# Optimization experiments

Measured on AMD Instinct MI355X. Metric: run time of the kernel, lower is better.

The kernel has to match this reference:

```python
import jax, jax.numpy as jnp
import numpy as np

N = 50000   # num_node
E = 1600000 # edge_size (N * avg_degree 32)
B = 64      # batch, hardcoded via repeat(64,1,1) in the torch module


def setup_inputs() -> dict:
    key = jax.random.key(0)
    k = jax.random.split(key, 8)
    return {
        "t": jax.random.normal(k[0], (1,), dtype=jnp.float32),
        "input": jax.random.normal(k[1], (B, N), dtype=jnp.float32),
        "edge_i": jax.random.randint(k[2], (E,), 0, N, dtype=jnp.int32),
        "edge_j": jax.random.randint(k[3], (E,), 0, N, dtype=jnp.int32),
        "weight_react": jax.random.normal(k[4], (1, E), dtype=jnp.float32) / 10.0,
        "weight_diff": jax.random.normal(k[5], (1, E), dtype=jnp.float32) / 1000.0,
        "bias_reaction": jax.random.normal(k[6], (1, N), dtype=jnp.float32) / 10.0,
        "bias_diffusion": jax.random.normal(k[7], (1, N), dtype=jnp.float32) / 10.0,
    }


def _lap_matvec(x, w, src, dst, n):
    # W[src_e, dst_e] = w_e (duplicates coalesce by sum, as torch sparse_coo_tensor does)
    # L = diag(colsum(W)) - W ; returns x @ L^T applied batched: out[b, v] = (L x[b])[v]
    col = jax.ops.segment_sum(w, dst, num_segments=n)                 # [N] column sums
    msg = jax.ops.segment_sum(w[:, None] * x[:, dst].T, src,
                              num_segments=n)                          # [N, B]
    return col[None, :] * x - msg.T                                   # [B, N]


def reference(t, input, edge_i, edge_j, weight_react, weight_diff,
              bias_reaction, bias_diffusion):
    x = input                                                          # [B, N]
    n = x.shape[1]
    # reaction Laplacian uses edges (i -> j); diffusion uses transposed (j -> i)
    reaction = _lap_matvec(x, weight_react[0], edge_i, edge_j, n) + bias_reaction
    diffusion = _lap_matvec(x, weight_diff[0], edge_j, edge_i, n) + bias_diffusion
    # up and down both True: tanh(reaction) + diffusion + input
    return jnp.tanh(reaction) + diffusion + x
```

## Files before the change

### kernel.cpp

```cpp
#include <hip/hip_runtime.h>
#include <hip/hip_fp16.h>


#define BKT_SHIFT 7
#define BKT_NODES 128
#define RCAP 4608
#define RCAP2 4992
#define CH 4096
#define NBP 512

#define RFL(x) __builtin_amdgcn_readfirstlane(x)

__device__ __forceinline__ unsigned bf16_rne(float f) {
    unsigned u = __float_as_uint(f);
    unsigned rb = (u >> 16) & 1u;
    u += 0x7FFFu + rb;
    return u >> 16;
}
__device__ __forceinline__ float bf16_lo(int y) {
    return __uint_as_float(((unsigned)y) << 16);
}
__device__ __forceinline__ float bf16_hi(int y) {
    return __uint_as_float((unsigned)y & 0xFFFF0000u);
}

__global__ void transpose_kernel(const float* __restrict__ x, __half* __restrict__ xth,
                                 int* __restrict__ gcur, int ngcur, int N) {
    __shared__ float tile[64][65];
    int v0 = blockIdx.x * 64;
    int tx = threadIdx.x;
    int ty = threadIdx.y;
    int flat = blockIdx.x * 1024 + ty * 64 + tx;
    if (flat < ngcur) gcur[flat] = 0;
    if (v0 + tx < N) {
        for (int b = ty; b < 64; b += 16)
            tile[tx][b] = x[b * N + v0 + tx];
    }
    __syncthreads();
    for (int vl = ty; vl < 64; vl += 16) {
        int v = v0 + vl;
        if (v < N)
            xth[(size_t)v * 64 + tx] = __float2half(tile[vl][tx]);
    }
}

__global__ void __launch_bounds__(512) partition_kernel(
        const int* __restrict__ ei, const int* __restrict__ ej,
        const float* __restrict__ wr, const float* __restrict__ wd,
        int* __restrict__ gcur, int2* __restrict__ runs,
        int E, int NB) {
    __shared__ int cnt[2 * NBP];
    __shared__ int base_a[2 * NBP];
    __shared__ int gb[2 * NBP];
    __shared__ int2 buf[2 * CH];

    int tid = threadIdx.x;
    int e0 = blockIdx.x * CH;
    int ch_len = min(CH, E - e0);
    if (ch_len <= 0) return;

    int my_i[8], my_j[8];
    unsigned my_w[8];
    #pragma unroll
    for (int k = 0; k < 8; ++k) {
        int t = tid + k * 512;
        if (t < ch_len) {
            int e = e0 + t;
            my_i[k] = ei[e];
            my_j[k] = ej[e];
            my_w[k] = (bf16_rne(wr[e]) << 16) | bf16_rne(wd[e]);
        } else {
            my_i[k] = -1;
        }
    }

    for (int b = tid; b < 2 * NBP; b += 512) cnt[b] = 0;
    __syncthreads();
    #pragma unroll
    for (int k = 0; k < 8; ++k) {
        if (my_i[k] >= 0) {
            atomicAdd(&cnt[my_i[k] >> BKT_SHIFT], 1);
            atomicAdd(&cnt[NBP + (my_j[k] >> BKT_SHIFT)], 1);
        }
    }
    __syncthreads();
    if (tid < 64) {
        int carry = 0;
        #pragma unroll
        for (int c = 0; c < (2 * NBP) / 64; ++c) {
            int idx = c * 64 + tid;
            int val = cnt[idx];
            int scan = val;
            for (int off = 1; off < 64; off <<= 1) {
                int n = __shfl_up(scan, off, 64);
                if (tid >= off) scan += n;
            }
            int excl = scan - val + carry;
            base_a[idx] = excl;
            cnt[idx] = excl;
            carry += __shfl(scan, 63, 64);
        }
    }
    __syncthreads();
    #pragma unroll
    for (int k = 0; k < 8; ++k) {
        if (my_i[k] >= 0) {
            int i = my_i[k], j = my_j[k];
            unsigned wv = my_w[k];
            int b0 = i >> BKT_SHIFT;
            int p0 = atomicAdd(&cnt[b0], 1);
            buf[p0] = make_int2((int)(((unsigned)b0 << 23) | ((unsigned)(i & 127) << 16) | (unsigned)j),
                                (int)wv);
            int b1 = j >> BKT_SHIFT;
            int p1 = atomicAdd(&cnt[NBP + b1], 1);
            buf[p1] = make_int2((int)(((unsigned)b1 << 23) | ((unsigned)(j & 127) << 16) | (unsigned)i),
                                (int)((wv << 16) | (wv >> 16)));
        }
    }
    __syncthreads();
    for (int cb = tid; cb < 2 * NBP; cb += 512) {
        int n = cnt[cb] - base_a[cb];
        if (n > 0) {
            int side = cb >> 9;
            int bkt = cb & (NBP - 1);
            gb[cb] = atomicAdd(&gcur[side * NB + bkt], n);
        }
    }
    __syncthreads();
    int total = 2 * ch_len;
    for (int t = tid; t < total; t += 512) {
        int2 p = buf[t];
        int side = (t >= ch_len) ? 1 : 0;
        int bkt = ((unsigned)p.x >> 23) & 0x1FF;
        int cb = side * NBP + bkt;
        int rank = gb[cb] + (t - base_a[cb]);
        if (rank < RCAP)
            runs[((size_t)(side * NB + bkt)) * RCAP + rank] = p;
    }
}

__global__ void __launch_bounds__(512) sortgather_kernel(
        const int* __restrict__ gcur, const int2* __restrict__ runs,
        const __half* __restrict__ xth,
        __half* __restrict__ msg, float* __restrict__ colsum,
        int NB, int N) {
    __shared__ int cnt[BKT_NODES];
    __shared__ int cur[BKT_NODES];
    __shared__ int pb[BKT_NODES];
    __shared__ float csum[BKT_NODES];
    __shared__ int dst[RCAP2];

    int sb = blockIdx.x;
    int side = (sb >= NB) ? 1 : 0;
    int b = sb - side * NB;
    int v0 = b << BKT_SHIFT;
    int len = min(gcur[sb], RCAP);
    size_t roff = (size_t)sb * RCAP;
    int tid = threadIdx.x;

    if (tid < BKT_NODES) { cnt[tid] = 0; csum[tid] = 0.f; }
    __syncthreads();
    for (int k = tid; k < len; k += 512) {
        int2 p = runs[roff + k];
        int dl = ((unsigned)p.x >> 16) & 0x7F;
        atomicAdd(&cnt[dl], 1);
        atomicAdd(&csum[dl], bf16_lo(p.y));
    }
    __syncthreads();
    if (tid < 64) {
        int carry = 0;
        #pragma unroll
        for (int c = 0; c < BKT_NODES / 64; ++c) {
            int idx = c * 64 + tid;
            int val = (cnt[idx] + 3) & ~3;
            int scan = val;
            for (int off = 1; off < 64; off <<= 1) {
                int n = __shfl_up(scan, off, 64);
                if (tid >= off) scan += n;
            }
            int excl = scan - val + carry;
            pb[idx] = excl;
            cur[idx] = excl;
            carry += __shfl(scan, 63, 64);
        }
    }
    __syncthreads();
    if (tid < BKT_NODES) {
        int pc = (cnt[tid] + 3) & ~3;
        for (int t = cnt[tid]; t < pc; ++t) dst[pb[tid] + t] = 0;
    }
    __syncthreads();
    for (int k = tid; k < len; k += 512) {
        int2 p = runs[roff + k];
        int dl = ((unsigned)p.x >> 16) & 0x7F;
        int pos = atomicAdd(&cur[dl], 1);
        dst[pos] = (int)(((unsigned)p.y & 0xFFFF0000u) | ((unsigned)p.x & 0xFFFFu));
    }
    __syncthreads();

    const unsigned* __restrict__ xth2 = (const unsigned*)xth;
    int lane = tid & 63;
    int halfl = lane & 31;
    int hi = lane >> 5;
    int wid = tid >> 6;
    for (int t = 0; t < BKT_NODES / 8; ++t) {
        int dl = wid * (BKT_NODES / 8) + t;
        int v = v0 + dl;
        if (v >= N) continue;
        const int* pay = dst + pb[dl] + hi;
        int npair = ((cnt[dl] + 3) & ~3) >> 1;
        float a0 = 0.f, a1 = 0.f;
        int q = 0;
        for (; q + 4 <= npair; q += 4) {
            int pA = pay[2 * q];
            int pB = pay[2 * q + 2];
            int pC = pay[2 * q + 4];
            int pD = pay[2 * q + 6];
            unsigned dA = xth2[(((size_t)((unsigned)pA & 0xFFFFu)) << 5) + halfl];
            unsigned dB = xth2[(((size_t)((unsigned)pB & 0xFFFFu)) << 5) + halfl];
            unsigned dC = xth2[(((size_t)((unsigned)pC & 0xFFFFu)) << 5) + halfl];
            unsigned dD = xth2[(((size_t)((unsigned)pD & 0xFFFFu)) << 5) + halfl];
            float wA = bf16_hi(pA), wB = bf16_hi(pB);
            float wC = bf16_hi(pC), wD = bf16_hi(pD);
            float2 xA = __half22float2(*(const __half2*)&dA);
            float2 xB = __half22float2(*(const __half2*)&dB);
            float2 xC = __half22float2(*(const __half2*)&dC);
            float2 xD = __half22float2(*(const __half2*)&dD);
            a0 = fmaf(wA, xA.x, a0); a1 = fmaf(wA, xA.y, a1);
            a0 = fmaf(wB, xB.x, a0); a1 = fmaf(wB, xB.y, a1);
            a0 = fmaf(wC, xC.x, a0); a1 = fmaf(wC, xC.y, a1);
            a0 = fmaf(wD, xD.x, a0); a1 = fmaf(wD, xD.y, a1);
        }
        for (; q < npair; ++q) {
            int p = pay[2 * q];
            unsigned d = xth2[(((size_t)((unsigned)p & 0xFFFFu)) << 5) + halfl];
            float wv = bf16_hi(p);
            float2 xf = __half22float2(*(const __half2*)&d);
            a0 = fmaf(wv, xf.x, a0);
            a1 = fmaf(wv, xf.y, a1);
        }
        a0 += __shfl_xor(a0, 32);
        a1 += __shfl_xor(a1, 32);
        if (hi == 0) {
            __half2 h = __floats2half2_rn(a0, a1);
            *(__half2*)(msg + ((size_t)side * N + v) * 64 + 2 * halfl) = h;
        }
        if (lane == 0)
            colsum[(size_t)side * N + v] = csum[dl];
    }
}

__global__ void final_kernel(const float* __restrict__ x,
                             const __half* __restrict__ msg,
                             const float* __restrict__ colsum,
                             const float* __restrict__ br, const float* __restrict__ bd,
                             float* __restrict__ out, int N) {
    __shared__ float tr[64][65];
    __shared__ float td[64][65];
    int v0 = blockIdx.x * 64;
    int tx = threadIdx.x;
    int ty = threadIdx.y;
    for (int vl = ty; vl < 64; vl += 16) {
        int v = v0 + vl;
        if (v < N) {
            tr[vl][tx] = __half2float(msg[(size_t)v * 64 + tx]);
            td[vl][tx] = __half2float(msg[((size_t)N + v) * 64 + tx]);
        }
    }
    __syncthreads();
    int v = v0 + tx;
    if (v < N) {
        float cold = colsum[v];
        float colr = colsum[(size_t)N + v];
        float brv = br[v], bdv = bd[v];
        for (int b = ty; b < 64; b += 16) {
            float xv = x[b * N + v];
            float r = colr * xv - tr[tx][b] + brv;
            float d = cold * xv - td[tx][b] + bdv;
            out[b * N + v] = tanhf(r) + d + xv;
        }
    }
}

extern "C" void kernel_launch(void* const* d_in, const int* in_sizes, int n_in,
                              void* d_out, int out_size, void* d_ws, size_t ws_size,
                              hipStream_t stream) {
    const float* x  = (const float*)d_in[1];
    const int*   ei = (const int*)d_in[2];
    const int*   ej = (const int*)d_in[3];
    const float* wr = (const float*)d_in[4];
    const float* wd = (const float*)d_in[5];
    const float* br = (const float*)d_in[6];
    const float* bd = (const float*)d_in[7];
    float* out = (float*)d_out;

    int E = in_sizes[2];
    int N = in_sizes[6];
    int NB = (N + BKT_NODES - 1) >> BKT_SHIFT;
    (void)out_size; (void)ws_size; (void)n_in;

    char* w = (char*)d_ws;
    __half* xth = (__half*)w;    w += (size_t)N * 64 * 2;
    __half* msg = (__half*)w;    w += (size_t)2 * N * 64 * 2;
    float* colsum = (float*)w;   w += (size_t)2 * N * 4;
    int* gcur   = (int*)w;       w += (size_t)2 * NB * 4;
    w = (char*)(((uintptr_t)w + 15) & ~(uintptr_t)15);
    int2* runs  = (int2*)w;

    dim3 tb(64, 16);
    int ntiles = (N + 63) / 64;
    transpose_kernel<<<ntiles, tb, 0, stream>>>(x, xth, gcur, 2 * NB, N);

    int nchunks = (E + CH - 1) / CH;
    partition_kernel<<<nchunks, 512, 0, stream>>>(ei, ej, wr, wd, gcur, runs, E, NB);

    sortgather_kernel<<<2 * NB, 512, 0, stream>>>(gcur, runs, xth, msg, colsum, NB, N);

    final_kernel<<<ntiles, tb, 0, stream>>>(x, msg, colsum, br, bd, out, N);
}
```

Baseline: 203.4 us.

## Widen gather to 16-byte loads with 8 edges per wave and cache runs in registers

The per-node gather now has each 8-lane group fetch a full 128-byte fp16 row with uint4 loads, so a wave handles 8 edges at once instead of 2. The 8 partial sums are combined with three xor-shuffles. Edge segments are padded to multiples of 8, and the shared dst buffer grows to hold the extra padding. The run entries are also loaded once into a 9-element register array instead of being read from global memory twice. This raises register pressure and adds some padding work on zero-weight entries.

Result: no change. 205.0 us (+0.8%).

```diff
diff --git a/kernel.cpp b/kernel.cpp
--- a/kernel.cpp
+++ b/kernel.cpp
@@ -5,7 +5,7 @@
 #define BKT_SHIFT 7
 #define BKT_NODES 128
 #define RCAP 4608
-#define RCAP2 4992
+#define RCAP2 5504
 #define CH 4096
 #define NBP 512
 
@@ -139,6 +139,22 @@
     }
 }
 
+#define ACC8(P, D)                                                        \
+    {                                                                     \
+        float wv_ = bf16_hi(P);                                           \
+        float2 f_;                                                        \
+        f_ = __half22float2(*(const __half2*)&(D).x);                     \
+        a0 = fmaf(wv_, f_.x, a0); a1 = fmaf(wv_, f_.y, a1);               \
+        f_ = __half22float2(*(const __half2*)&(D).y);                     \
+        a2 = fmaf(wv_, f_.x, a2); a3 = fmaf(wv_, f_.y, a3);               \
+        f_ = __half22float2(*(const __half2*)&(D).z);                     \
+        a4 = fmaf(wv_, f_.x, a4); a5 = fmaf(wv_, f_.y, a5);               \
+        f_ = __half22float2(*(const __half2*)&(D).w);                     \
+        a6 = fmaf(wv_, f_.x, a6); a7 = fmaf(wv_, f_.y, a7);               \
+    }
+
+#define COMB3(A) { A += __shfl_xor(A, 8); A += __shfl_xor(A, 16); A += __shfl_xor(A, 32); }
+
 __global__ void __launch_bounds__(512) sortgather_kernel(
         const int* __restrict__ gcur, const int2* __restrict__ runs,
         const __half* __restrict__ xth,
@@ -158,13 +174,23 @@
     size_t roff = (size_t)sb * RCAP;
     int tid = threadIdx.x;
 
+    int2 my[9];
+    #pragma unroll
+    for (int k = 0; k < 9; ++k) {
+        int t = tid + k * 512;
+        if (t < len) my[k] = runs[roff + t];
+        else my[k].x = -1;
+    }
+
     if (tid < BKT_NODES) { cnt[tid] = 0; csum[tid] = 0.f; }
     __syncthreads();
-    for (int k = tid; k < len; k += 512) {
-        int2 p = runs[roff + k];
-        int dl = ((unsigned)p.x >> 16) & 0x7F;
-        atomicAdd(&cnt[dl], 1);
-        atomicAdd(&csum[dl], bf16_lo(p.y));
+    #pragma unroll
+    for (int k = 0; k < 9; ++k) {
+        if (my[k].x != -1) {
+            int dl = ((unsigned)my[k].x >> 16) & 0x7F;
+            atomicAdd(&cnt[dl], 1);
+            atomicAdd(&csum[dl], bf16_lo(my[k].y));
+        }
     }
     __syncthreads();
     if (tid < 64) {
@@ -172,7 +198,7 @@
         #pragma unroll
         for (int c = 0; c < BKT_NODES / 64; ++c) {
             int idx = c * 64 + tid;
-            int val = (cnt[idx] + 3) & ~3;
+            int val = (cnt[idx] + 7) & ~7;
             int scan = val;
             for (int off = 1; off < 64; off <<= 1) {
                 int n = __shfl_up(scan, off, 64);
@@ -186,64 +212,63 @@
     }
     __syncthreads();
     if (tid < BKT_NODES) {
-        int pc = (cnt[tid] + 3) & ~3;
+        int pc = (cnt[tid] + 7) & ~7;
         for (int t = cnt[tid]; t < pc; ++t) dst[pb[tid] + t] = 0;
     }
     __syncthreads();
-    for (int k = tid; k < len; k += 512) {
-        int2 p = runs[roff + k];
-        int dl = ((unsigned)p.x >> 16) & 0x7F;
-        int pos = atomicAdd(&cur[dl], 1);
-        dst[pos] = (int)(((unsigned)p.y & 0xFFFF0000u) | ((unsigned)p.x & 0xFFFFu));
-    }
-    __syncthreads();
-
-    const unsigned* __restrict__ xth2 = (const unsigned*)xth;
+    #pragma unroll
+    for (int k = 0; k < 9; ++k) {
+        if (my[k].x != -1) {
+            int dl = ((unsigned)my[k].x >> 16) & 0x7F;
+            int pos = atomicAdd(&cur[dl], 1);
+            dst[pos] = (int)(((unsigned)my[k].y & 0xFFFF0000u) | ((unsigned)my[k].x & 0xFFFFu));
+        }
+    }
+    __syncthreads();
+
+    const uint4* __restrict__ xq = (const uint4*)xth;
     int lane = tid & 63;
-    int halfl = lane & 31;
-    int hi = lane >> 5;
+    int g  = lane >> 3;
+    int bl = lane & 7;
     int wid = tid >> 6;
     for (int t = 0; t < BKT_NODES / 8; ++t) {
         int dl = wid * (BKT_NODES / 8) + t;
         int v = v0 + dl;
         if (v >= N) continue;
-        const int* pay = dst + pb[dl] + hi;
-        int npair = ((cnt[dl] + 3) & ~3) >> 1;
-        float a0 = 0.f, a1 = 0.f;
-        int q = 0;
-        for (; q + 4 <= npair; q += 4) {
-            int pA = pay[2 * q];
-            int pB = pay[2 * q + 2];
-            int pC = pay[2 * q + 4];
-            int pD = pay[2 * q + 6];
-            unsigned dA = xth2[(((size_t)((unsigned)pA & 0xFFFFu)) << 5) + halfl];
-            unsigned dB = xth2[(((size_t)((unsigned)pB & 0xFFFFu)) << 5) + halfl];
-            unsigned dC = xth2[(((size_t)((unsigned)pC & 0xFFFFu)) << 5) + halfl];
-            unsigned dD = xth2[(((size_t)((unsigned)pD & 0xFFFFu)) << 5) + halfl];
-            float wA = bf16_hi(pA), wB = bf16_hi(pB);
-            float wC = bf16_hi(pC), wD = bf16_hi(pD);
-            float2 xA = __half22float2(*(const __half2*)&dA);
-            float2 xB = __half22float2(*(const __half2*)&dB);
-            float2 xC = __half22float2(*(const __half2*)&dC);
-            float2 xD = __half22float2(*(const __half2*)&dD);
-            a0 = fmaf(wA, xA.x, a0); a1 = fmaf(wA, xA.y, a1);
-            a0 = fmaf(wB, xB.x, a0); a1 = fmaf(wB, xB.y, a1);
-            a0 = fmaf(wC, xC.x, a0); a1 = fmaf(wC, xC.y, a1);
-            a0 = fmaf(wD, xD.x, a0); a1 = fmaf(wD, xD.y, a1);
-        }
-        for (; q < npair; ++q) {
-            int p = pay[2 * q];
-            unsigned d = xth2[(((size_t)((unsigned)p & 0xFFFFu)) << 5) + halfl];
-            float wv = bf16_hi(p);
-            float2 xf = __half22float2(*(const __half2*)&d);
-            a0 = fmaf(wv, xf.x, a0);
-            a1 = fmaf(wv, xf.y, a1);
-        }
-        a0 += __shfl_xor(a0, 32);
-        a1 += __shfl_xor(a1, 32);
-        if (hi == 0) {
-            __half2 h = __floats2half2_rn(a0, a1);
-            *(__half2*)(msg + ((size_t)side * N + v) * 64 + 2 * halfl) = h;
+        const int* pay = dst + pb[dl] + g;
+        int noct = ((cnt[dl] + 7) & ~7) >> 3;
+        float a0 = 0.f, a1 = 0.f, a2 = 0.f, a3 = 0.f;
+        float a4 = 0.f, a5 = 0.f, a6 = 0.f, a7 = 0.f;
+        int o = 0;
+        for (; o + 4 <= noct; o += 4) {
+            int pA = pay[8 * o];
+            int pB = pay[8 * o + 8];
+            int pC = pay[8 * o + 16];
+            int pD = pay[8 * o + 24];
+            uint4 dA = xq[(((size_t)((unsigned)pA & 0xFFFFu)) << 3) + bl];
+            uint4 dB = xq[(((size_t)((unsigned)pB & 0xFFFFu)) << 3) + bl];
+            uint4 dC = xq[(((size_t)((unsigned)pC & 0xFFFFu)) << 3) + bl];
+            uint4 dD = xq[(((size_t)((unsigned)pD & 0xFFFFu)) << 3) + bl];
+            ACC8(pA, dA)
+            ACC8(pB, dB)
+            ACC8(pC, dC)
+            ACC8(pD, dD)
+        }
+        for (; o < noct; ++o) {
+            int p = pay[8 * o];
+            uint4 d = xq[(((size_t)((unsigned)p & 0xFFFFu)) << 3) + bl];
+            ACC8(p, d)
+        }
+        COMB3(a0) COMB3(a1) COMB3(a2) COMB3(a3)
+        COMB3(a4) COMB3(a5) COMB3(a6) COMB3(a7)
+        if (lane < 8) {
+            __half2 h0 = __floats2half2_rn(a0, a1);
+            __half2 h1 = __floats2half2_rn(a2, a3);
+            __half2 h2 = __floats2half2_rn(a4, a5);
+            __half2 h3 = __floats2half2_rn(a6, a7);
+            uint4 st = make_uint4(*(unsigned*)&h0, *(unsigned*)&h1,
+                                  *(unsigned*)&h2, *(unsigned*)&h3);
+            *(uint4*)(msg + ((size_t)side * N + v) * 64 + 8 * lane) = st;
         }
         if (lane == 0)
             colsum[(size_t)side * N + v] = csum[dl];
```
